# Performance work log

Measured on AMD Instinct MI355X. Metric: run time of the kernel, lower is better.

The kernel has to match this reference:

```python
import jax, jax.numpy as jnp
import numpy as np

IN_F = 256
OUT_F = 512
DEG = 3
BATCH = 2048


def setup_inputs() -> dict:
    key = jax.random.key(0)
    k_x, k_p, k_q, k_w = jax.random.split(key, 4)
    x = jax.random.normal(k_x, (BATCH, IN_F), dtype=jnp.float32)
    P_coef = jax.random.normal(k_p, (OUT_F, IN_F, DEG + 1), dtype=jnp.float32) * 0.1
    Q_coef = jax.random.normal(k_q, (OUT_F, IN_F, DEG), dtype=jnp.float32) * 0.1
    # reset_parameters(): constant term of P zeroed, constant of Q set to 1
    P_coef = P_coef.at[:, :, 0].set(0.0)
    Q_coef = Q_coef.at[:, :, 0].set(1.0)
    # xavier_uniform for base_weight
    limit = float(np.sqrt(6.0 / (IN_F + OUT_F)))
    base_weight = jax.random.uniform(k_w, (OUT_F, IN_F), dtype=jnp.float32,
                                     minval=-limit, maxval=limit)
    base_bias = jnp.zeros((OUT_F,), dtype=jnp.float32)
    return {"x": x, "P_coef": P_coef, "Q_coef": Q_coef,
            "base_weight": base_weight, "base_bias": base_bias}


def reference(x, P_coef, Q_coef, base_weight, base_bias):
    # x: (B, I). Powers x^0..x^DEG -> (B, I, DEG+1)
    exps = jnp.arange(DEG + 1, dtype=x.dtype)
    x_powers = x[..., None] ** exps  # (B, I, P)
    # P[b,i,o] = sum_p P_coef[o,i,p] * x[b,i]^p
    P = jnp.einsum('oip,bip->bio', P_coef, x_powers)
    # Q uses powers x^1..x^DEG
    Q = 1.0 + jnp.einsum('oip,bip->bio', Q_coef, x_powers[:, :, 1:])
    rational = P / (Q + 1e-6)          # (B, I, O)
    rational_output = rational.sum(axis=1)  # (B, O)
    base_output = x @ base_weight.T + base_bias  # (B, O)
    return base_output + rational_output
```

## Files before the change

### kernel.cpp

```cpp
#include <hip/hip_runtime.h>

constexpr int IN_F  = 256;
constexpr int OUT_F = 512;
constexpr int BATCH = 2048;

__global__ __launch_bounds__(256) void prep_pack8_kernel(
    const float* __restrict__ p, const float* __restrict__ q,
    const float* __restrict__ w, float4* __restrict__ pk, int n) {
    int t = blockIdx.x * 256 + threadIdx.x;
    if (t < n) {
        pk[2 * t]     = make_float4(p[4 * t], p[4 * t + 1], p[4 * t + 2], p[4 * t + 3]);
        pk[2 * t + 1] = make_float4(q[3 * t], q[3 * t + 1], q[3 * t + 2], w[t]);
    }
}

__global__ __launch_bounds__(256) void prep_x3_kernel(
    const float* __restrict__ x, float* __restrict__ x3, int n) {
    int t = blockIdx.x * 256 + threadIdx.x;
    if (t < n) {
        const double xd = (double)x[t];
        x3[t] = (float)(xd * xd * xd);
    }
}

template <int MODE>
__global__ __launch_bounds__(256, 8) void kan_kernel(
    const float*  __restrict__ x,
    const float4* __restrict__ Pc,
    const float*  __restrict__ Qc,
    const float4* __restrict__ PK,
    const float*  __restrict__ X3,
    const float*  __restrict__ W,
    const float*  __restrict__ bias,
    float* __restrict__ out)
{
#pragma clang fp contract(off)
    const int lane  = threadIdx.x & 63;
    const int wave  = __builtin_amdgcn_readfirstlane(threadIdx.x >> 6);
    const int b     = blockIdx.x * 64 + lane;
    const int o0    = blockIdx.y * 8;
    const int ibase = wave * 64;

    float acc[8] = {0.f, 0.f, 0.f, 0.f, 0.f, 0.f, 0.f, 0.f};
    const float* xrow  = x + (size_t)b * IN_F + ibase;
    const float* x3row = (MODE == 2) ? (X3 + (size_t)b * IN_F + ibase) : nullptr;

#pragma unroll 2
    for (int ic = 0; ic < 64; ic += 4) {
        const float4 xq = *reinterpret_cast<const float4*>(xrow + ic);
        float x1[4] = {xq.x, xq.y, xq.z, xq.w};
        float x2[4], x3v[4];
        if (MODE == 2) {
            const float4 x3q = *reinterpret_cast<const float4*>(x3row + ic);
            x3v[0] = x3q.x; x3v[1] = x3q.y; x3v[2] = x3q.z; x3v[3] = x3q.w;
#pragma unroll
            for (int j = 0; j < 4; ++j) x2[j] = x1[j] * x1[j];
        } else {
#pragma unroll
            for (int j = 0; j < 4; ++j) {
                x2[j] = x1[j] * x1[j];
                const double xd = (double)x1[j];
                x3v[j] = (float)(xd * xd * xd);
            }
        }
        const int rowi = ibase + ic;
#pragma unroll
        for (int oo = 0; oo < 8; ++oo) {
            const int rowbase = (o0 + oo) * IN_F + rowi;
#pragma unroll
            for (int j = 0; j < 4; ++j) {
                float p0, p1, p2, p3, q1, q2, q3, wv;
                if (MODE >= 1) {
                    const float4 pa = PK[2 * (size_t)(rowbase + j)];
                    const float4 pb = PK[2 * (size_t)(rowbase + j) + 1];
                    p0 = pa.x; p1 = pa.y; p2 = pa.z; p3 = pa.w;
                    q1 = pb.x; q2 = pb.y; q3 = pb.z; wv = pb.w;
                } else {
                    const float4 pc = Pc[rowbase + j];
                    const float* qp = Qc + (size_t)(rowbase + j) * 3;
                    p0 = pc.x; p1 = pc.y; p2 = pc.z; p3 = pc.w;
                    q1 = qp[0]; q2 = qp[1]; q3 = qp[2];
                    wv = W[rowbase + j];
                }
                float t = q1 * x1[j];
                t = fmaf(q2, x2[j], t);
                t = fmaf(q3, x3v[j], t);
                float Qv = 1.0f + t;
                float Qp = Qv + 1e-6f;
                float s = fmaf(p1, x1[j], p0);
                s = fmaf(p2, x2[j], s);
                s = fmaf(p3, x3v[j], s);
                const float r = __builtin_amdgcn_rcpf(Qp);
                acc[oo] = fmaf(s, r, acc[oo]);
                acc[oo] = fmaf(wv, x1[j], acc[oo]);
            }
        }
    }

    __shared__ float red[4 * 64 * 9];
    {
        float* dst = &red[(wave * 64 + lane) * 9];
#pragma unroll
        for (int v = 0; v < 8; ++v) dst[v] = acc[v];
    }
    __syncthreads();

#pragma unroll
    for (int k = 0; k < 2; ++k) {
        const int idx = threadIdx.x + k * 256;
        const int bb = idx >> 3, o = idx & 7;
        const int e = bb * 9 + o;
        float s = red[e] + red[576 + e];
        s = s + red[1152 + e];
        s = s + red[1728 + e];
        s = s + bias[o0 + o];
        out[(size_t)(blockIdx.x * 64 + bb) * OUT_F + o0 + o] = s;
    }
}

extern "C" void kernel_launch(void* const* d_in, const int* in_sizes, int n_in,
                              void* d_out, int out_size, void* d_ws, size_t ws_size,
                              hipStream_t stream) {
    const float* x    = (const float*)d_in[0];
    const float* Pc   = (const float*)d_in[1];
    const float* Qc   = (const float*)d_in[2];
    const float* W    = (const float*)d_in[3];
    const float* bias = (const float*)d_in[4];
    float* out = (float*)d_out;

    const int n  = OUT_F * IN_F;
    const int nx = BATCH * IN_F;
    const size_t pk_bytes = (size_t)n * 32;
    dim3 grid(BATCH / 64, OUT_F / 8);

    if (ws_size >= pk_bytes + (size_t)nx * sizeof(float)) {
        float4* pk = (float4*)d_ws;
        float*  x3 = (float*)((char*)d_ws + pk_bytes);
        prep_pack8_kernel<<<(n + 255) / 256, 256, 0, stream>>>(Pc, Qc, W, pk, n);
        prep_x3_kernel<<<(nx + 255) / 256, 256, 0, stream>>>(x, x3, nx);
        kan_kernel<2><<<grid, 256, 0, stream>>>(
            x, (const float4*)Pc, Qc, pk, x3, W, bias, out);
    } else if (ws_size >= pk_bytes) {
        float4* pk = (float4*)d_ws;
        prep_pack8_kernel<<<(n + 255) / 256, 256, 0, stream>>>(Pc, Qc, W, pk, n);
        kan_kernel<1><<<grid, 256, 0, stream>>>(
            x, (const float4*)Pc, Qc, pk, nullptr, W, bias, out);
    } else {
        kan_kernel<0><<<grid, 256, 0, stream>>>(
            x, (const float4*)Pc, Qc, nullptr, nullptr, W, bias, out);
    }
}
```

Before: 120.2 us.

## Retile main kernel to 128 batch rows by 4 outputs per block

Adds a dedicated kernel for the packed-coefficient path. Each thread now handles two batch rows and four outputs instead of one row and eight outputs, so every coefficient record loaded from memory is reused across two rows. Coefficient loads are grouped as four consecutive float4s covering two input features. The change aims to cut coefficient traffic per FLOP, at the cost of twice the x/x3 loads per thread and a different grid shape.

```diff
diff --git a/kernel.cpp b/kernel.cpp
--- a/kernel.cpp
+++ b/kernel.cpp
@@ -23,16 +23,118 @@
     }
 }
 
+__global__ __launch_bounds__(256, 8) void kan2_kernel(
+    const float*  __restrict__ x,
+    const float4* __restrict__ PK,
+    const float*  __restrict__ X3,
+    const float*  __restrict__ bias,
+    float* __restrict__ out)
+{
+#pragma clang fp contract(off)
+    const int lane  = threadIdx.x & 63;
+    const int wave  = __builtin_amdgcn_readfirstlane(threadIdx.x >> 6);
+    const int bA    = blockIdx.x * 128 + lane;
+    const int o0    = blockIdx.y * 4;
+    const int ibase = wave * 64;
+
+    float accA[4] = {0.f, 0.f, 0.f, 0.f};
+    float accB[4] = {0.f, 0.f, 0.f, 0.f};
+    const float* xrowA  = x  + (size_t)bA * IN_F + ibase;
+    const float* xrowB  = xrowA + (size_t)64 * IN_F;
+    const float* x3rowA = X3 + (size_t)bA * IN_F + ibase;
+    const float* x3rowB = x3rowA + (size_t)64 * IN_F;
+
+    for (int ic = 0; ic < 64; ic += 4) {
+        const float4 xqA  = *reinterpret_cast<const float4*>(xrowA + ic);
+        const float4 x3qA = *reinterpret_cast<const float4*>(x3rowA + ic);
+        const float4 xqB  = *reinterpret_cast<const float4*>(xrowB + ic);
+        const float4 x3qB = *reinterpret_cast<const float4*>(x3rowB + ic);
+        float x1A[4] = {xqA.x, xqA.y, xqA.z, xqA.w};
+        float x3A[4] = {x3qA.x, x3qA.y, x3qA.z, x3qA.w};
+        float x1B[4] = {xqB.x, xqB.y, xqB.z, xqB.w};
+        float x3B[4] = {x3qB.x, x3qB.y, x3qB.z, x3qB.w};
+        float x2A[4], x2B[4];
+#pragma unroll
+        for (int j = 0; j < 4; ++j) {
+            x2A[j] = x1A[j] * x1A[j];
+            x2B[j] = x1B[j] * x1B[j];
+        }
+        const int rowi = ibase + ic;
+#pragma unroll
+        for (int oo = 0; oo < 4; ++oo) {
+            const size_t base = 2 * ((size_t)(o0 + oo) * IN_F + rowi);
+#pragma unroll
+            for (int jp = 0; jp < 2; ++jp) {
+                const float4* rec = PK + base + 4 * jp;
+                const float4 r0 = rec[0];
+                const float4 r1 = rec[1];
+                const float4 r2 = rec[2];
+                const float4 r3 = rec[3];
+#pragma unroll
+                for (int h = 0; h < 2; ++h) {
+                    const int j = 2 * jp + h;
+                    const float4 cp = h ? r2 : r0;
+                    const float4 cq = h ? r3 : r1;
+                    {
+                        float t = cq.x * x1A[j];
+                        t = fmaf(cq.y, x2A[j], t);
+                        t = fmaf(cq.z, x3A[j], t);
+                        float Qv = 1.0f + t;
+                        float Qp = Qv + 1e-6f;
+                        float s = fmaf(cp.y, x1A[j], cp.x);
+                        s = fmaf(cp.z, x2A[j], s);
+                        s = fmaf(cp.w, x3A[j], s);
+                        const float r = __builtin_amdgcn_rcpf(Qp);
+                        accA[oo] = fmaf(s, r, accA[oo]);
+                        accA[oo] = fmaf(cq.w, x1A[j], accA[oo]);
+                    }
+                    {
+                        float t = cq.x * x1B[j];
+                        t = fmaf(cq.y, x2B[j], t);
+                        t = fmaf(cq.z, x3B[j], t);
+                        float Qv = 1.0f + t;
+                        float Qp = Qv + 1e-6f;
+                        float s = fmaf(cp.y, x1B[j], cp.x);
+                        s = fmaf(cp.z, x2B[j], s);
+                        s = fmaf(cp.w, x3B[j], s);
+                        const float r = __builtin_amdgcn_rcpf(Qp);
+                        accB[oo] = fmaf(s, r, accB[oo]);
+                        accB[oo] = fmaf(cq.w, x1B[j], accB[oo]);
+                    }
+                }
+            }
+        }
+    }
+
+    __shared__ float red[4 * 64 * 9];
+    {
+        float* dst = &red[(wave * 64 + lane) * 9];
+#pragma unroll
+        for (int v = 0; v < 4; ++v) dst[v] = accA[v];
+#pragma unroll
+        for (int v = 0; v < 4; ++v) dst[4 + v] = accB[v];
+    }
+    __syncthreads();
+
+#pragma unroll
+    for (int k = 0; k < 2; ++k) {
+        const int f  = threadIdx.x + k * 256;
+        const int bb = f >> 2, o = f & 3;
+        const int e  = (bb & 63) * 9 + (bb >> 6) * 4 + o;
+        float s = red[e] + red[576 + e];
+        s = s + red[1152 + e];
+        s = s + red[1728 + e];
+        s = s + bias[o0 + o];
+        out[(size_t)(blockIdx.x * 128 + bb) * OUT_F + o0 + o] = s;
+    }
+}
+
 template <int MODE>
 __global__ __launch_bounds__(256, 8) void kan_kernel(
     const float*  __restrict__ x,
-    const float4* __restrict__ Pc,
-    const float*  __restrict__ Qc,
-    const float4* __restrict__ PK,
-    const float*  __restrict__ X3,
-    const float*  __restrict__ W,
-    const float*  __restrict__ bias,
-    float* __restrict__ out)
+    const float4* __restrict__ Pc, const float* __restrict__ Qc,
+    const float4* __restrict__ PK, const float* __restrict__ W,
+    const float* __restrict__ bias, float* __restrict__ out)
 {
 #pragma clang fp contract(off)
     const int lane  = threadIdx.x & 63;
@@ -42,26 +144,17 @@
     const int ibase = wave * 64;
 
     float acc[8] = {0.f, 0.f, 0.f, 0.f, 0.f, 0.f, 0.f, 0.f};
-    const float* xrow  = x + (size_t)b * IN_F + ibase;
-    const float* x3row = (MODE == 2) ? (X3 + (size_t)b * IN_F + ibase) : nullptr;
-
-#pragma unroll 2
+    const float* xrow = x + (size_t)b * IN_F + ibase;
+
     for (int ic = 0; ic < 64; ic += 4) {
         const float4 xq = *reinterpret_cast<const float4*>(xrow + ic);
         float x1[4] = {xq.x, xq.y, xq.z, xq.w};
         float x2[4], x3v[4];
-        if (MODE == 2) {
-            const float4 x3q = *reinterpret_cast<const float4*>(x3row + ic);
-            x3v[0] = x3q.x; x3v[1] = x3q.y; x3v[2] = x3q.z; x3v[3] = x3q.w;
-#pragma unroll
-            for (int j = 0; j < 4; ++j) x2[j] = x1[j] * x1[j];
-        } else {
-#pragma unroll
-            for (int j = 0; j < 4; ++j) {
-                x2[j] = x1[j] * x1[j];
-                const double xd = (double)x1[j];
-                x3v[j] = (float)(xd * xd * xd);
-            }
+#pragma unroll
+        for (int j = 0; j < 4; ++j) {
+            x2[j] = x1[j] * x1[j];
+            const double xd = (double)x1[j];
+            x3v[j] = (float)(xd * xd * xd);
         }
         const int rowi = ibase + ic;
 #pragma unroll
@@ -70,7 +163,7 @@
 #pragma unroll
             for (int j = 0; j < 4; ++j) {
                 float p0, p1, p2, p3, q1, q2, q3, wv;
-                if (MODE >= 1) {
+                if (MODE == 1) {
                     const float4 pa = PK[2 * (size_t)(rowbase + j)];
                     const float4 pb = PK[2 * (size_t)(rowbase + j) + 1];
                     p0 = pa.x; p1 = pa.y; p2 = pa.z; p3 = pa.w;
@@ -104,7 +197,6 @@
         for (int v = 0; v < 8; ++v) dst[v] = acc[v];
     }
     __syncthreads();
-
 #pragma unroll
     for (int k = 0; k < 2; ++k) {
         const int idx = threadIdx.x + k * 256;
@@ -131,22 +223,23 @@
     const int n  = OUT_F * IN_F;
     const int nx = BATCH * IN_F;
     const size_t pk_bytes = (size_t)n * 32;
-    dim3 grid(BATCH / 64, OUT_F / 8);
 
     if (ws_size >= pk_bytes + (size_t)nx * sizeof(float)) {
         float4* pk = (float4*)d_ws;
         float*  x3 = (float*)((char*)d_ws + pk_bytes);
         prep_pack8_kernel<<<(n + 255) / 256, 256, 0, stream>>>(Pc, Qc, W, pk, n);
         prep_x3_kernel<<<(nx + 255) / 256, 256, 0, stream>>>(x, x3, nx);
-        kan_kernel<2><<<grid, 256, 0, stream>>>(
-            x, (const float4*)Pc, Qc, pk, x3, W, bias, out);
+        dim3 grid(BATCH / 128, OUT_F / 4);
+        kan2_kernel<<<grid, 256, 0, stream>>>(x, pk, x3, bias, out);
     } else if (ws_size >= pk_bytes) {
         float4* pk = (float4*)d_ws;
         prep_pack8_kernel<<<(n + 255) / 256, 256, 0, stream>>>(Pc, Qc, W, pk, n);
+        dim3 grid(BATCH / 64, OUT_F / 8);
         kan_kernel<1><<<grid, 256, 0, stream>>>(
-            x, (const float4*)Pc, Qc, pk, nullptr, W, bias, out);
+            x, (const float4*)Pc, Qc, pk, W, bias, out);
     } else {
+        dim3 grid(BATCH / 64, OUT_F / 8);
         kan_kernel<0><<<grid, 256, 0, stream>>>(
-            x, (const float4*)Pc, Qc, nullptr, nullptr, W, bias, out);
-    }
-}
+            x, (const float4*)Pc, Qc, nullptr, W, bias, out);
+    }
+}
```

Result: slower. 191.1 us (+59.0%).

## Stage packed coefficients into LDS with double-buffered async global_load_lds

Applied to the files above, without the earlier changes.

Adds a dedicated kernel that copies packed P/Q/W coefficient chunks for the block's 8 outputs into a double-buffered LDS arena using global_load_lds, prefetching the next chunk while computing the current one. Each wave then reads coefficients from LDS instead of issuing uniform global loads. This aims to hide global load latency and share coefficient fetches across waves, at the cost of a block barrier per chunk and extra LDS use.

```diff
diff --git a/kernel.cpp b/kernel.cpp
--- a/kernel.cpp
+++ b/kernel.cpp
@@ -23,14 +23,10 @@
     }
 }
 
-template <int MODE>
-__global__ __launch_bounds__(256, 8) void kan_kernel(
+__global__ __launch_bounds__(256, 8) void kan3_kernel(
     const float*  __restrict__ x,
-    const float4* __restrict__ Pc,
-    const float*  __restrict__ Qc,
     const float4* __restrict__ PK,
     const float*  __restrict__ X3,
-    const float*  __restrict__ W,
     const float*  __restrict__ bias,
     float* __restrict__ out)
 {
@@ -41,27 +37,117 @@
     const int o0    = blockIdx.y * 8;
     const int ibase = wave * 64;
 
+    __shared__ float4 arena4[576];
+
+    const int sub  = lane >> 1;
+    const int half = lane & 1;
+    const int s_oo = 2 * wave + (sub >> 4);
+    const int s_wv = (sub & 15) >> 2;
+    const int s_jj = sub & 3;
+    const char* src = (const char*)PK
+        + (((size_t)(o0 + s_oo) * IN_F + 64 * s_wv + s_jj) * 32) + half * 16;
+
     float acc[8] = {0.f, 0.f, 0.f, 0.f, 0.f, 0.f, 0.f, 0.f};
-    const float* xrow  = x + (size_t)b * IN_F + ibase;
-    const float* x3row = (MODE == 2) ? (X3 + (size_t)b * IN_F + ibase) : nullptr;
-
-#pragma unroll 2
+    const float* xrow  = x  + (size_t)b * IN_F + ibase;
+    const float* x3row = X3 + (size_t)b * IN_F + ibase;
+
+    {
+        float4* dst = &arena4[0 * 256 + wave * 64];
+        __builtin_amdgcn_global_load_lds(
+            (const __attribute__((address_space(1))) void*)src,
+            (__attribute__((address_space(3))) void*)dst, 16, 0, 0);
+    }
+    __syncthreads();
+
+    int par = 0;
+    for (int c = 0; c < 16; ++c) {
+        if (c < 15) {
+            const char* s = src + (size_t)(c + 1) * 128;
+            float4* dst = &arena4[(par ^ 1) * 256 + wave * 64];
+            __builtin_amdgcn_global_load_lds(
+                (const __attribute__((address_space(1))) void*)s,
+                (__attribute__((address_space(3))) void*)dst, 16, 0, 0);
+        }
+        const float4 xq  = *reinterpret_cast<const float4*>(xrow  + 4 * c);
+        const float4 x3q = *reinterpret_cast<const float4*>(x3row + 4 * c);
+        float x1[4]  = {xq.x, xq.y, xq.z, xq.w};
+        float x3v[4] = {x3q.x, x3q.y, x3q.z, x3q.w};
+        float x2[4];
+#pragma unroll
+        for (int j = 0; j < 4; ++j) x2[j] = x1[j] * x1[j];
+
+        const float4* tile = &arena4[par * 256];
+#pragma unroll
+        for (int oo = 0; oo < 8; ++oo) {
+#pragma unroll
+            for (int j = 0; j < 4; ++j) {
+                const int ent = oo * 16 + wave * 4 + j;
+                const float4 cp = tile[2 * ent];
+                const float4 cq = tile[2 * ent + 1];
+                float t = cq.x * x1[j];
+                t = fmaf(cq.y, x2[j], t);
+                t = fmaf(cq.z, x3v[j], t);
+                float Qv = 1.0f + t;
+                float Qp = Qv + 1e-6f;
+                float s = fmaf(cp.y, x1[j], cp.x);
+                s = fmaf(cp.z, x2[j], s);
+                s = fmaf(cp.w, x3v[j], s);
+                const float r = __builtin_amdgcn_rcpf(Qp);
+                acc[oo] = fmaf(s, r, acc[oo]);
+                acc[oo] = fmaf(cq.w, x1[j], acc[oo]);
+            }
+        }
+        __syncthreads();
+        par ^= 1;
+    }
+
+    float* red = (float*)arena4;
+    {
+        float* dst = &red[(wave * 64 + lane) * 9];
+#pragma unroll
+        for (int v = 0; v < 8; ++v) dst[v] = acc[v];
+    }
+    __syncthreads();
+
+#pragma unroll
+    for (int k = 0; k < 2; ++k) {
+        const int idx = threadIdx.x + k * 256;
+        const int bb = idx >> 3, o = idx & 7;
+        const int e = bb * 9 + o;
+        float s = red[e] + red[576 + e];
+        s = s + red[1152 + e];
+        s = s + red[1728 + e];
+        s = s + bias[o0 + o];
+        out[(size_t)(blockIdx.x * 64 + bb) * OUT_F + o0 + o] = s;
+    }
+}
+
+template <int MODE>
+__global__ __launch_bounds__(256, 8) void kan_kernel(
+    const float*  __restrict__ x,
+    const float4* __restrict__ Pc, const float* __restrict__ Qc,
+    const float4* __restrict__ PK, const float* __restrict__ W,
+    const float* __restrict__ bias, float* __restrict__ out)
+{
+#pragma clang fp contract(off)
+    const int lane  = threadIdx.x & 63;
+    const int wave  = __builtin_amdgcn_readfirstlane(threadIdx.x >> 6);
+    const int b     = blockIdx.x * 64 + lane;
+    const int o0    = blockIdx.y * 8;
+    const int ibase = wave * 64;
+
+    float acc[8] = {0.f, 0.f, 0.f, 0.f, 0.f, 0.f, 0.f, 0.f};
+    const float* xrow = x + (size_t)b * IN_F + ibase;
+
     for (int ic = 0; ic < 64; ic += 4) {
         const float4 xq = *reinterpret_cast<const float4*>(xrow + ic);
         float x1[4] = {xq.x, xq.y, xq.z, xq.w};
         float x2[4], x3v[4];
-        if (MODE == 2) {
-            const float4 x3q = *reinterpret_cast<const float4*>(x3row + ic);
-            x3v[0] = x3q.x; x3v[1] = x3q.y; x3v[2] = x3q.z; x3v[3] = x3q.w;
-#pragma unroll
-            for (int j = 0; j < 4; ++j) x2[j] = x1[j] * x1[j];
-        } else {
-#pragma unroll
-            for (int j = 0; j < 4; ++j) {
-                x2[j] = x1[j] * x1[j];
-                const double xd = (double)x1[j];
-                x3v[j] = (float)(xd * xd * xd);
-            }
+#pragma unroll
+        for (int j = 0; j < 4; ++j) {
+            x2[j] = x1[j] * x1[j];
+            const double xd = (double)x1[j];
+            x3v[j] = (float)(xd * xd * xd);
         }
         const int rowi = ibase + ic;
 #pragma unroll
@@ -70,7 +156,7 @@
 #pragma unroll
             for (int j = 0; j < 4; ++j) {
                 float p0, p1, p2, p3, q1, q2, q3, wv;
-                if (MODE >= 1) {
+                if (MODE == 1) {
                     const float4 pa = PK[2 * (size_t)(rowbase + j)];
                     const float4 pb = PK[2 * (size_t)(rowbase + j) + 1];
                     p0 = pa.x; p1 = pa.y; p2 = pa.z; p3 = pa.w;
@@ -104,7 +190,6 @@
         for (int v = 0; v < 8; ++v) dst[v] = acc[v];
     }
     __syncthreads();
-
 #pragma unroll
     for (int k = 0; k < 2; ++k) {
         const int idx = threadIdx.x + k * 256;
@@ -138,15 +223,14 @@
         float*  x3 = (float*)((char*)d_ws + pk_bytes);
         prep_pack8_kernel<<<(n + 255) / 256, 256, 0, stream>>>(Pc, Qc, W, pk, n);
         prep_x3_kernel<<<(nx + 255) / 256, 256, 0, stream>>>(x, x3, nx);
-        kan_kernel<2><<<grid, 256, 0, stream>>>(
-            x, (const float4*)Pc, Qc, pk, x3, W, bias, out);
+        kan3_kernel<<<grid, 256, 0, stream>>>(x, pk, x3, bias, out);
     } else if (ws_size >= pk_bytes) {
         float4* pk = (float4*)d_ws;
         prep_pack8_kernel<<<(n + 255) / 256, 256, 0, stream>>>(Pc, Qc, W, pk, n);
         kan_kernel<1><<<grid, 256, 0, stream>>>(
-            x, (const float4*)Pc, Qc, pk, nullptr, W, bias, out);
+            x, (const float4*)Pc, Qc, pk, W, bias, out);
     } else {
         kan_kernel<0><<<grid, 256, 0, stream>>>(
-            x, (const float4*)Pc, Qc, nullptr, nullptr, W, bias, out);
-    }
-}
+            x, (const float4*)Pc, Qc, nullptr, W, bias, out);
+    }
+}
```

New measurement: 172.6 us. 43.6% more time.

## Add per-thread full-K kernel with wave-uniform coefficient loads, drop LDS reduction

Applied to the files above, without the earlier changes.

Adds a new main kernel in which each thread owns one batch row and two outputs and loops over all 256 inputs. This removes the cross-wave shared-memory reduction and the __syncthreads barrier. Within a block all lanes share the same output columns, so coefficient loads are uniform across the wave and can be broadcast. The trade-off is less reuse of x per coefficient load: two outputs per thread instead of eight, and longer serial loops. The old kernel's MODE 2 path is removed.

```diff
diff --git a/kernel.cpp b/kernel.cpp
--- a/kernel.cpp
+++ b/kernel.cpp
@@ -23,16 +23,66 @@
     }
 }
 
+__global__ __launch_bounds__(256, 8) void kan4_kernel(
+    const float*  __restrict__ x,
+    const float4* __restrict__ PK,
+    const float*  __restrict__ X3,
+    const float*  __restrict__ bias,
+    float* __restrict__ out)
+{
+#pragma clang fp contract(off)
+    const int lane = threadIdx.x & 63;
+    const int wave = __builtin_amdgcn_readfirstlane(threadIdx.x >> 6);
+    const int ot   = blockIdx.x & 255;
+    const int bb   = blockIdx.x >> 8;
+    const int o0   = ot * 2;
+    const int b    = bb * 256 + wave * 64 + lane;
+
+    float acc[2] = {0.f, 0.f};
+    const float* xrow  = x  + (size_t)b * IN_F;
+    const float* x3row = X3 + (size_t)b * IN_F;
+
+    for (int ic = 0; ic < IN_F; ic += 4) {
+        const float4 xq  = *reinterpret_cast<const float4*>(xrow  + ic);
+        const float4 x3q = *reinterpret_cast<const float4*>(x3row + ic);
+        float x1[4]  = {xq.x, xq.y, xq.z, xq.w};
+        float x3v[4] = {x3q.x, x3q.y, x3q.z, x3q.w};
+        float x2[4];
+#pragma unroll
+        for (int j = 0; j < 4; ++j) x2[j] = x1[j] * x1[j];
+
+#pragma unroll
+        for (int oo = 0; oo < 2; ++oo) {
+            const int rowbase = (o0 + oo) * IN_F + ic;
+#pragma unroll
+            for (int j = 0; j < 4; ++j) {
+                const float4 cp = PK[2 * (size_t)(rowbase + j)];
+                const float4 cq = PK[2 * (size_t)(rowbase + j) + 1];
+                float t = cq.x * x1[j];
+                t = fmaf(cq.y, x2[j], t);
+                t = fmaf(cq.z, x3v[j], t);
+                float Qv = 1.0f + t;
+                float Qp = Qv + 1e-6f;
+                float s = fmaf(cp.y, x1[j], cp.x);
+                s = fmaf(cp.z, x2[j], s);
+                s = fmaf(cp.w, x3v[j], s);
+                const float r = __builtin_amdgcn_rcpf(Qp);
+                acc[oo] = fmaf(s, r, acc[oo]);
+                acc[oo] = fmaf(cq.w, x1[j], acc[oo]);
+            }
+        }
+    }
+
+    float2 res = make_float2(acc[0] + bias[o0], acc[1] + bias[o0 + 1]);
+    *reinterpret_cast<float2*>(out + (size_t)b * OUT_F + o0) = res;
+}
+
 template <int MODE>
 __global__ __launch_bounds__(256, 8) void kan_kernel(
     const float*  __restrict__ x,
-    const float4* __restrict__ Pc,
-    const float*  __restrict__ Qc,
-    const float4* __restrict__ PK,
-    const float*  __restrict__ X3,
-    const float*  __restrict__ W,
-    const float*  __restrict__ bias,
-    float* __restrict__ out)
+    const float4* __restrict__ Pc, const float* __restrict__ Qc,
+    const float4* __restrict__ PK, const float* __restrict__ W,
+    const float* __restrict__ bias, float* __restrict__ out)
 {
 #pragma clang fp contract(off)
     const int lane  = threadIdx.x & 63;
@@ -42,26 +92,17 @@
     const int ibase = wave * 64;
 
     float acc[8] = {0.f, 0.f, 0.f, 0.f, 0.f, 0.f, 0.f, 0.f};
-    const float* xrow  = x + (size_t)b * IN_F + ibase;
-    const float* x3row = (MODE == 2) ? (X3 + (size_t)b * IN_F + ibase) : nullptr;
+    const float* xrow = x + (size_t)b * IN_F + ibase;
 
-#pragma unroll 2
     for (int ic = 0; ic < 64; ic += 4) {
         const float4 xq = *reinterpret_cast<const float4*>(xrow + ic);
         float x1[4] = {xq.x, xq.y, xq.z, xq.w};
         float x2[4], x3v[4];
-        if (MODE == 2) {
-            const float4 x3q = *reinterpret_cast<const float4*>(x3row + ic);
-            x3v[0] = x3q.x; x3v[1] = x3q.y; x3v[2] = x3q.z; x3v[3] = x3q.w;
 #pragma unroll
-            for (int j = 0; j < 4; ++j) x2[j] = x1[j] * x1[j];
-        } else {
-#pragma unroll
-            for (int j = 0; j < 4; ++j) {
-                x2[j] = x1[j] * x1[j];
-                const double xd = (double)x1[j];
-                x3v[j] = (float)(xd * xd * xd);
-            }
+        for (int j = 0; j < 4; ++j) {
+            x2[j] = x1[j] * x1[j];
+            const double xd = (double)x1[j];
+            x3v[j] = (float)(xd * xd * xd);
         }
         const int rowi = ibase + ic;
 #pragma unroll
@@ -70,7 +111,7 @@
 #pragma unroll
             for (int j = 0; j < 4; ++j) {
                 float p0, p1, p2, p3, q1, q2, q3, wv;
-                if (MODE >= 1) {
+                if (MODE == 1) {
                     const float4 pa = PK[2 * (size_t)(rowbase + j)];
                     const float4 pb = PK[2 * (size_t)(rowbase + j) + 1];
                     p0 = pa.x; p1 = pa.y; p2 = pa.z; p3 = pa.w;
@@ -104,7 +145,6 @@
         for (int v = 0; v < 8; ++v) dst[v] = acc[v];
     }
     __syncthreads();
-
 #pragma unroll
     for (int k = 0; k < 2; ++k) {
         const int idx = threadIdx.x + k * 256;
@@ -131,22 +171,22 @@
     const int n  = OUT_F * IN_F;
     const int nx = BATCH * IN_F;
     const size_t pk_bytes = (size_t)n * 32;
-    dim3 grid(BATCH / 64, OUT_F / 8);
 
     if (ws_size >= pk_bytes + (size_t)nx * sizeof(float)) {
         float4* pk = (float4*)d_ws;
         float*  x3 = (float*)((char*)d_ws + pk_bytes);
         prep_pack8_kernel<<<(n + 255) / 256, 256, 0, stream>>>(Pc, Qc, W, pk, n);
         prep_x3_kernel<<<(nx + 255) / 256, 256, 0, stream>>>(x, x3, nx);
-        kan_kernel<2><<<grid, 256, 0, stream>>>(
-            x, (const float4*)Pc, Qc, pk, x3, W, bias, out);
+        kan4_kernel<<<dim3(2048), 256, 0, stream>>>(x, pk, x3, bias, out);
     } else if (ws_size >= pk_bytes) {
         float4* pk = (float4*)d_ws;
         prep_pack8_kernel<<<(n + 255) / 256, 256, 0, stream>>>(Pc, Qc, W, pk, n);
+        dim3 grid(BATCH / 64, OUT_F / 8);
         kan_kernel<1><<<grid, 256, 0, stream>>>(
-            x, (const float4*)Pc, Qc, pk, nullptr, W, bias, out);
+            x, (const float4*)Pc, Qc, pk, W, bias, out);
     } else {
+        dim3 grid(BATCH / 64, OUT_F / 8);
         kan_kernel<0><<<grid, 256, 0, stream>>>(
-            x, (const float4*)Pc, Qc, nullptr, nullptr, W, bias, out);
+            x, (const float4*)Pc, Qc, nullptr, W, bias, out);
     }
 }
```

Result: slower. 266.8 us (+121.9%).
